# Kernel tuning notes

Measured on AMD Instinct MI355X. Metric: run time of the kernel, lower is better.

## Reference

```python
import jax, jax.numpy as jnp
import numpy as np

B, S, D, H, DK, DV = 2, 2048, 1024, 16, 64, 64
EPS = 1e-6

def setup_inputs() -> dict:
    key = jax.random.key(0)
    ks = jax.random.split(key, 5)
    sc = 1.0 / np.sqrt(D)
    return {
        "ip": jax.random.normal(ks[0], (B, S, D), jnp.float32),
        "wk": jax.random.normal(ks[1], (D, H * DK), jnp.float32) * sc,
        "wq": jax.random.normal(ks[2], (D, H * DK), jnp.float32) * sc,
        "wv": jax.random.normal(ks[3], (D, H * DV), jnp.float32) * sc,
        "fc_w": jax.random.normal(ks[4], (H * DV, D), jnp.float32) * (1.0 / np.sqrt(H * DV)),
        "fc_b": jnp.zeros((D,), jnp.float32),
        "ln_g": jnp.ones((D,), jnp.float32),
        "ln_b": jnp.zeros((D,), jnp.float32),
    }

def reference(ip, wk, wq, wv, fc_w, fc_b, ln_g, ln_b):
    m, t, _ = ip.shape
    temp = jnp.asarray(DK ** 0.5, ip.dtype)
    # projections -> [m, t, H, d]
    k = (ip @ wk).reshape(m, t, H, DK)
    q = (ip @ wq).reshape(m, t, H, DK)
    v = (ip @ wv).reshape(m, t, H, DV)
    # scores [m, H, t, t]; dropout is identity in eval mode
    scores = jnp.einsum('mqhd,mkhd->mhqk', q, k) / temp
    attn = jax.nn.softmax(scores, axis=-1)
    # context [m, t, H*DV]
    ctx = jnp.einsum('mhqk,mkhd->mqhd', attn, v).reshape(m, t, H * DV)
    out = ctx @ fc_w + fc_b + ip  # fc + residual
    # LayerNorm over last dim (biased variance, eps=1e-6)
    mu = jnp.mean(out, axis=-1, keepdims=True)
    var = jnp.mean(jnp.square(out - mu), axis=-1, keepdims=True)
    y = (out - mu) * jax.lax.rsqrt(var + EPS) * ln_g + ln_b
    return (y, attn)
```

## Files before the change

kernel.cpp:

```cpp
#include <hip/hip_runtime.h>
#include <hip/hip_bf16.h>
#include <stdint.h>

#define S_LEN 2048
#define DMODEL 1024
#define NH 16
#define HD 64
#define SC2 0.18033688011112042f

typedef __attribute__((ext_vector_type(8))) short bf16x8;
typedef __attribute__((ext_vector_type(4))) float f32x4;
typedef unsigned long long u64;

__device__ __forceinline__ void gload16(const void* g, void* l) {
  __builtin_amdgcn_global_load_lds(
      reinterpret_cast<const __attribute__((address_space(1))) void*>(reinterpret_cast<uintptr_t>(g)),
      reinterpret_cast<__attribute__((address_space(3))) void*>(reinterpret_cast<uintptr_t>(l)),
      16, 0, 0);
}

__device__ __forceinline__ f32x4 mfma_bf16(bf16x8 a, bf16x8 b, f32x4 c) {
  return __builtin_amdgcn_mfma_f32_16x16x32_bf16(a, b, c, 0, 0, 0);
}

__device__ __forceinline__ unsigned short bfbits(float x) {
  __hip_bfloat16 h = __float2bfloat16(x);
  return *reinterpret_cast<unsigned short*>(&h);
}

__device__ __forceinline__ float asf(unsigned u) {
  union { unsigned u; float f; } c; c.u = u; return c.f;
}

__device__ __forceinline__ void wait_vm0_bar() {
  __builtin_amdgcn_sched_barrier(0);
  asm volatile("s_waitcnt vmcnt(0) lgkmcnt(0)" ::: "memory");
  __builtin_amdgcn_s_barrier();
  __builtin_amdgcn_sched_barrier(0);
}
__device__ __forceinline__ void wait_vm2_bar() {
  __builtin_amdgcn_sched_barrier(0);
  asm volatile("s_waitcnt vmcnt(2) lgkmcnt(0)" ::: "memory");
  __builtin_amdgcn_s_barrier();
  __builtin_amdgcn_sched_barrier(0);
}
__device__ __forceinline__ void wait_vm4_bar() {
  __builtin_amdgcn_sched_barrier(0);
  asm volatile("s_waitcnt vmcnt(4) lgkmcnt(0)" ::: "memory");
  __builtin_amdgcn_s_barrier();
  __builtin_amdgcn_sched_barrier(0);
}

__global__ __launch_bounds__(256) void k_prep(const float* __restrict__ ip,
                                              const float* __restrict__ wq,
                                              const float* __restrict__ wk,
                                              const float* __restrict__ wv,
                                              const float* __restrict__ fcw,
                                              __hip_bfloat16* __restrict__ ipb,
                                              __hip_bfloat16* __restrict__ wt_all,
                                              __hip_bfloat16* __restrict__ fct) {
  int bid = blockIdx.x;
  if (bid < 4096) {
    int i = (bid * 256 + threadIdx.x) * 4;
    f32x4 v = *(const f32x4*)(ip + i);
    u64 p = (u64)bfbits(v[0]) | ((u64)bfbits(v[1]) << 16) | ((u64)bfbits(v[2]) << 32)
          | ((u64)bfbits(v[3]) << 48);
    *reinterpret_cast<u64*>(ipb + i) = p;
    return;
  }
  bid -= 4096;
  const int z = bid >> 10, tile_id = bid & 1023;
  const float* src = (z == 0) ? wq : (z == 1) ? wk : (z == 2) ? wv : fcw;
  __hip_bfloat16* dst = (z == 3) ? fct : wt_all + (size_t)z * DMODEL * DMODEL;
  __shared__ float tile[32][33];
  const int nb = (tile_id & 31) * 32, kb = (tile_id >> 5) * 32;
  const int lx = threadIdx.x & 31, ly = threadIdx.x >> 5;
#pragma unroll
  for (int i = 0; i < 4; ++i)
    tile[ly + 8 * i][lx] = src[(size_t)(kb + ly + 8 * i) * DMODEL + nb + lx];
  __syncthreads();
#pragma unroll
  for (int i = 0; i < 4; ++i)
    dst[(size_t)(nb + ly + 8 * i) * DMODEL + kb + lx] = __float2bfloat16(tile[lx][ly + 8 * i]);
}

__global__ __launch_bounds__(1024) void k_transpose_v(const unsigned short* __restrict__ V,
                                                      unsigned short* __restrict__ Vt) {
  __shared__ unsigned short tile[32][33];
  const int bh = blockIdx.z;
  const int sb = blockIdx.x * 32, db = blockIdx.y * 32;
  const unsigned short* src = V + (size_t)bh * S_LEN * HD;
  unsigned short* dst = Vt + (size_t)bh * HD * S_LEN;
  tile[threadIdx.y][threadIdx.x] = src[(size_t)(sb + threadIdx.y) * HD + db + threadIdx.x];
  __syncthreads();
  dst[(size_t)(db + threadIdx.y) * S_LEN + sb + threadIdx.x] = tile[threadIdx.x][threadIdx.y];
}

template <int MODE>
__global__ __launch_bounds__(256) void k_gemm(const __hip_bfloat16* __restrict__ A,
                                              const __hip_bfloat16* __restrict__ Bt,
                                              __hip_bfloat16* __restrict__ Q,
                                              __hip_bfloat16* __restrict__ Kk,
                                              __hip_bfloat16* __restrict__ V,
                                              const float* __restrict__ ipf,
                                              const float* __restrict__ bias,
                                              float* __restrict__ preln) {
  __shared__ __align__(128) char lds[16384];
  char* Al = lds;
  char* Bl = lds + 8192;
  const int t = threadIdx.x;
  const int w = t >> 6, l = t & 63;
  const int g = l >> 4, lr = l & 15;
  const int cpx = gridDim.x >> 3;
  const int swz = (blockIdx.x & 7) * cpx + (blockIdx.x >> 3);
  const int bm = swz & 31;
  const int bn = swz >> 5;

  int sr0 = (w * 2 + 0) * 16 + (l >> 2);
  int sr1 = (w * 2 + 1) * 16 + (l >> 2);
  const int sc = (l & 3) * 16;
  const char* aSrc0 = (const char*)A + ((size_t)(bm * 128 + sr0)) * 2048 + (sc ^ (((sr0 >> 1) & 3) << 4));
  const char* aSrc1 = (const char*)A + ((size_t)(bm * 128 + sr1)) * 2048 + (sc ^ (((sr1 >> 1) & 3) << 4));
  const char* bSrc0 = (const char*)Bt + ((size_t)(bn * 128 + sr0)) * 2048 + (sc ^ (((sr0 >> 1) & 3) << 4));
  const char* bSrc1 = (const char*)Bt + ((size_t)(bn * 128 + sr1)) * 2048 + (sc ^ (((sr1 >> 1) & 3) << 4));

  const int wm = (w >> 1) * 64, wn = (w & 1) * 64;
  int roff[4], noff[4];
#pragma unroll
  for (int mi = 0; mi < 4; ++mi) {
    int m = wm + mi * 16 + lr;
    roff[mi] = m * 64 + ((g * 16) ^ (((m >> 1) & 3) << 4));
  }
#pragma unroll
  for (int ni = 0; ni < 4; ++ni) {
    int n = wn + ni * 16 + lr;
    noff[ni] = n * 64 + ((g * 16) ^ (((n >> 1) & 3) << 4));
  }

  f32x4 acc[4][4] = {};
  for (int k0 = 0; k0 < DMODEL; k0 += 32) {
    gload16(aSrc0 + k0 * 2, Al + (w * 2 + 0) * 1024);
    gload16(aSrc1 + k0 * 2, Al + (w * 2 + 1) * 1024);
    gload16(bSrc0 + k0 * 2, Bl + (w * 2 + 0) * 1024);
    gload16(bSrc1 + k0 * 2, Bl + (w * 2 + 1) * 1024);
    __syncthreads();
    bf16x8 af[4], bfv[4];
#pragma unroll
    for (int mi = 0; mi < 4; ++mi) af[mi] = *(const bf16x8*)(Al + roff[mi]);
#pragma unroll
    for (int ni = 0; ni < 4; ++ni) bfv[ni] = *(const bf16x8*)(Bl + noff[ni]);
#pragma unroll
    for (int mi = 0; mi < 4; ++mi)
#pragma unroll
      for (int ni = 0; ni < 4; ++ni)
        acc[mi][ni] = mfma_bf16(af[mi], bfv[ni], acc[mi][ni]);
    __syncthreads();
  }

#pragma unroll
  for (int mi = 0; mi < 4; ++mi)
#pragma unroll
    for (int ni = 0; ni < 4; ++ni) {
      f32x4 v = acc[mi][ni];
#pragma unroll
      for (int r = 0; r < 4; ++r) {
        int m = bm * 128 + wm + mi * 16 + g * 4 + r;
        int n = bn * 128 + wn + ni * 16 + lr;
        if (MODE == 0) {
          int mat = n >> 10, c = n & 1023;
          int h = c >> 6, d = c & 63;
          int b = m >> 11, s = m & 2047;
          size_t idx = (((size_t)(b * NH + h)) * S_LEN + s) * HD + d;
          __hip_bfloat16 hv = __float2bfloat16(v[r]);
          if (mat == 0) Q[idx] = hv;
          else if (mat == 1) Kk[idx] = hv;
          else V[idx] = hv;
        } else {
          size_t idx = (size_t)m * DMODEL + n;
          preln[idx] = v[r] + bias[n] + ipf[idx];
        }
      }
    }
}

__global__ __launch_bounds__(256, 2) void k_attn8(const __hip_bfloat16* __restrict__ Q,
                                                  const __hip_bfloat16* __restrict__ K,
                                                  const __hip_bfloat16* __restrict__ Vt,
                                                  float* __restrict__ attn,
                                                  __hip_bfloat16* __restrict__ ctx) {
  __shared__ __align__(128) char KVst[4][8192];
  __shared__ __align__(128) char Pw[2][4][4096];

  const int t = threadIdx.x, w = t >> 6, l = t & 63;
  const int g = l >> 4, lr = l & 15;
  const int bid = blockIdx.x;
  const int bh = bid & 31, qi = bid >> 5;
  const int b = bh >> 4, h = bh & 15;
  const int q0 = qi * 64 + w * 16;
  const char* Kh = (const char*)(K + (size_t)bh * S_LEN * HD);
  const char* Vh = (const char*)(Vt + (size_t)bh * HD * S_LEN);
  const __hip_bfloat16* Qh = Q + (size_t)bh * S_LEN * HD;

  bf16x8 qf0 = *(const bf16x8*)(Qh + (size_t)(q0 + lr) * HD + 8 * g);
  bf16x8 qf1 = *(const bf16x8*)(Qh + (size_t)(q0 + lr) * HD + 32 + 8 * g);

  const int srow0 = w * 8 + (l >> 3), srow1 = srow0 + 32;
  const int sb = (l & 7) * 16;
  const int kso0 = srow0 * 128 + (sb ^ ((srow0 & 7) << 4));
  const int kso1 = srow1 * 128 + (sb ^ ((srow1 & 7) << 4));
  const int vso0 = srow0 * 4096 + (sb ^ ((srow0 & 7) << 4));
  const int vso1 = srow1 * 4096 + (sb ^ ((srow1 & 7) << 4));
  const int swz = (lr & 7) << 4;

  gload16(Kh + kso0, &KVst[0][w * 1024]);
  gload16(Kh + kso1, &KVst[0][4096 + w * 1024]);
  gload16(Kh + 8192 + kso0, &KVst[1][w * 1024]);
  gload16(Kh + 8192 + kso1, &KVst[1][4096 + w * 1024]);
  float lsum = 0.f;
#define P1_COMPUTE(c)                                                              \
  {                                                                                \
    const char* kb_ = &KVst[(c) & 3][0];                                           \
    _Pragma("unroll") for (int st = 0; st < 4; ++st) {                             \
      const char* kr = kb_ + (st * 16 + lr) * 128;                                 \
      bf16x8 kf0 = *(const bf16x8*)(kr + ((g * 16) ^ swz));                        \
      bf16x8 kf1 = *(const bf16x8*)(kr + ((64 + g * 16) ^ swz));                   \
      f32x4 s = {};                                                                \
      s = mfma_bf16(kf0, qf0, s);                                                  \
      s = mfma_bf16(kf1, qf1, s);                                                  \
      lsum += __builtin_amdgcn_exp2f(s[0] * SC2) + __builtin_amdgcn_exp2f(s[1] * SC2) \
            + __builtin_amdgcn_exp2f(s[2] * SC2) + __builtin_amdgcn_exp2f(s[3] * SC2); \
    }                                                                              \
  }
  for (int c = 0; c < 30; ++c) {
    gload16(Kh + (c + 2) * 8192 + kso0, &KVst[(c + 2) & 3][w * 1024]);
    gload16(Kh + (c + 2) * 8192 + kso1, &KVst[(c + 2) & 3][4096 + w * 1024]);
    wait_vm4_bar();
    P1_COMPUTE(c);
  }
  wait_vm2_bar();
  P1_COMPUTE(30);
  wait_vm0_bar();
  P1_COMPUTE(31);
#undef P1_COMPUTE
  lsum += __shfl_xor(lsum, 16);
  lsum += __shfl_xor(lsum, 32);
  const float inv = 1.0f / lsum;

  gload16(Kh + kso0, &KVst[0][w * 1024]);
  gload16(Kh + kso1, &KVst[0][4096 + w * 1024]);
  gload16(Vh + vso0, &KVst[2][w * 1024]);
  gload16(Vh + vso1, &KVst[2][4096 + w * 1024]);
  wait_vm0_bar();

  f32x4 o[4] = {};
  const size_t arowbase = ((size_t)bh * S_LEN + q0) * S_LEN;
  const int sl_row = l >> 5, sl_col = l & 31;
  for (int c = 0; c < 32; ++c) {
    const int cur = c & 1;
    const int gbuf = (c >> 1) & 1;
    const int ce = c & 1;
    if (c < 31) {
      gload16(Kh + (c + 1) * 8192 + kso0, &KVst[cur ^ 1][w * 1024]);
      gload16(Kh + (c + 1) * 8192 + kso1, &KVst[cur ^ 1][4096 + w * 1024]);
      gload16(Vh + (c + 1) * 128 + vso0, &KVst[2 + (cur ^ 1)][w * 1024]);
      gload16(Vh + (c + 1) * 128 + vso1, &KVst[2 + (cur ^ 1)][4096 + w * 1024]);
    }
    if (c >= 2) {
      const char* psrc = &Pw[gbuf ^ 1][w][0];
      const int kvb = ((c >> 1) - 1) * 128;
#pragma unroll
      for (int i = 0; i < 4; ++i) {
        int row = ce * 8 + 2 * i + sl_row;
        u64 v = *reinterpret_cast<const u64*>(psrc + row * 256 + ((sl_col * 8) ^ ((row & 7) << 4)));
        unsigned lo = (unsigned)v, hi = (unsigned)(v >> 32);
        f32x4 pv;
        pv[0] = asf(lo << 16);
        pv[1] = asf(lo & 0xffff0000u);
        pv[2] = asf(hi << 16);
        pv[3] = asf(hi & 0xffff0000u);
        __builtin_nontemporal_store(pv, (f32x4*)(attn + arowbase + (size_t)row * S_LEN + kvb + sl_col * 4));
      }
    }
#pragma unroll
    for (int st = 0; st < 4; ++st) {
      const char* kr = &KVst[cur][(st * 16 + lr) * 128];
      bf16x8 kf0 = *(const bf16x8*)(kr + ((g * 16) ^ swz));
      bf16x8 kf1 = *(const bf16x8*)(kr + ((64 + g * 16) ^ swz));
      f32x4 s = {};
      s = mfma_bf16(kf0, qf0, s);
      s = mfma_bf16(kf1, qf1, s);
      float p0 = __builtin_amdgcn_exp2f(s[0] * SC2) * inv;
      float p1 = __builtin_amdgcn_exp2f(s[1] * SC2) * inv;
      float p2 = __builtin_amdgcn_exp2f(s[2] * SC2) * inv;
      float p3 = __builtin_amdgcn_exp2f(s[3] * SC2) * inv;
      u64 u = (u64)bfbits(p0) | ((u64)bfbits(p1) << 16) | ((u64)bfbits(p2) << 32)
            | ((u64)bfbits(p3) << 48);
      *reinterpret_cast<u64*>(&Pw[gbuf][w][lr * 256 + ((ce * 128 + st * 32 + g * 8) ^ swz)]) = u;
    }
#pragma unroll
    for (int ks = 0; ks < 2; ++ks) {
      bf16x8 pf = *(const bf16x8*)(&Pw[gbuf][w][lr * 256 + ((ce * 128 + ks * 64 + g * 16) ^ swz)]);
#pragma unroll
      for (int dvt = 0; dvt < 4; ++dvt) {
        const char* vb = &KVst[2 + cur][(dvt * 16 + lr) * 128];
        bf16x8 vf = *(const bf16x8*)(vb + ((ks * 64 + g * 16) ^ swz));
        o[dvt] = mfma_bf16(pf, vf, o[dvt]);
      }
    }
    if (c < 31) wait_vm4_bar();
  }

  {
    const char* psrc = &Pw[1][w][0];
#pragma unroll
    for (int i = 0; i < 8; ++i) {
      int row = 2 * i + sl_row;
      u64 v = *reinterpret_cast<const u64*>(psrc + row * 256 + ((sl_col * 8) ^ ((row & 7) << 4)));
      unsigned lo = (unsigned)v, hi = (unsigned)(v >> 32);
      f32x4 pv;
      pv[0] = asf(lo << 16);
      pv[1] = asf(lo & 0xffff0000u);
      pv[2] = asf(hi << 16);
      pv[3] = asf(hi & 0xffff0000u);
      __builtin_nontemporal_store(pv, (f32x4*)(attn + arowbase + (size_t)row * S_LEN + 1920 + sl_col * 4));
    }
  }

#pragma unroll
  for (int dvt = 0; dvt < 4; ++dvt)
#pragma unroll
    for (int r = 0; r < 4; ++r) {
      int q = q0 + g * 4 + r;
      size_t idx = ((size_t)b * S_LEN + q) * DMODEL + h * HD + dvt * 16 + lr;
      ctx[idx] = __float2bfloat16(o[dvt][r]);
    }
}

__global__ __launch_bounds__(256) void k_ln(const float* __restrict__ x,
                                            const float* __restrict__ gam,
                                            const float* __restrict__ bet,
                                            float* __restrict__ y) {
  const int row = blockIdx.x;
  const int i = threadIdx.x * 4;
  const float* xr = x + (size_t)row * DMODEL;
  f32x4 v = *(const f32x4*)(xr + i);
  float s = v[0] + v[1] + v[2] + v[3];
  float s2 = v[0] * v[0] + v[1] * v[1] + v[2] * v[2] + v[3] * v[3];
#pragma unroll
  for (int off = 1; off < 64; off <<= 1) {
    s += __shfl_xor(s, off);
    s2 += __shfl_xor(s2, off);
  }
  __shared__ float red[2][4];
  const int w = threadIdx.x >> 6, ln = threadIdx.x & 63;
  if (ln == 0) { red[0][w] = s; red[1][w] = s2; }
  __syncthreads();
  s = red[0][0] + red[0][1] + red[0][2] + red[0][3];
  s2 = red[1][0] + red[1][1] + red[1][2] + red[1][3];
  const float mu = s * (1.f / DMODEL);
  const float rstd = rsqrtf(s2 * (1.f / DMODEL) - mu * mu + 1e-6f);
  f32x4 gv = *(const f32x4*)(gam + i), bv = *(const f32x4*)(bet + i);
  f32x4 out;
#pragma unroll
  for (int j = 0; j < 4; ++j) out[j] = (v[j] - mu) * rstd * gv[j] + bv[j];
  *(f32x4*)(y + (size_t)row * DMODEL + i) = out;
}

extern "C" void kernel_launch(void* const* d_in, const int* in_sizes, int n_in,
                              void* d_out, int out_size, void* d_ws, size_t ws_size,
                              hipStream_t stream) {
  const float* ip  = (const float*)d_in[0];
  const float* wk  = (const float*)d_in[1];
  const float* wq  = (const float*)d_in[2];
  const float* wv  = (const float*)d_in[3];
  const float* fcw = (const float*)d_in[4];
  const float* fcb = (const float*)d_in[5];
  const float* lng = (const float*)d_in[6];
  const float* lnb = (const float*)d_in[7];

  float* y = (float*)d_out;
  float* attn = y + (size_t)2 * S_LEN * DMODEL;

  char* ws = (char*)d_ws;
  __hip_bfloat16* ipb = (__hip_bfloat16*)(ws);
  __hip_bfloat16* wt  = (__hip_bfloat16*)(ws + (8ll << 20));
  __hip_bfloat16* fct = (__hip_bfloat16*)(ws + (14ll << 20));
  __hip_bfloat16* Qb  = (__hip_bfloat16*)(ws + (16ll << 20));
  __hip_bfloat16* Kb  = (__hip_bfloat16*)(ws + (24ll << 20));
  __hip_bfloat16* Vb  = (__hip_bfloat16*)(ws + (32ll << 20));
  __hip_bfloat16* Vtb = (__hip_bfloat16*)(ws + (40ll << 20));
  __hip_bfloat16* ctx = (__hip_bfloat16*)(ws + (48ll << 20));
  float* preln        = (float*)(ws + (56ll << 20));

  k_prep<<<8192, 256, 0, stream>>>(ip, wq, wk, wv, fcw, ipb, wt, fct);
  k_gemm<0><<<32 * 24, 256, 0, stream>>>(ipb, wt, Qb, Kb, Vb, nullptr, nullptr, nullptr);
  k_transpose_v<<<dim3(64, 2, 32), dim3(32, 32), 0, stream>>>((const unsigned short*)Vb,
                                                              (unsigned short*)Vtb);
  k_attn8<<<1024, 256, 0, stream>>>(Qb, Kb, Vtb, attn, ctx);
  k_gemm<1><<<32 * 8, 256, 0, stream>>>(ctx, fct, nullptr, nullptr, nullptr, ip, fcb, preln);
  k_ln<<<4096, 256, 0, stream>>>(preln, lng, lnb, y);
}
```

Measured before the change: 217.8 us.

## Fuse V transpose into QKV GEMM epilogue, read bf16 residual, raise MFMA priority

The QKV projection GEMM now writes V directly in transposed [bh, d, s] layout, packing four consecutive sequence elements into one 64-bit store. This removes the separate k_transpose_v kernel and its extra round trip through global memory. The output-projection GEMM reads the residual from the bf16 copy of the input instead of the fp32 original, halving that read but losing residual precision. The attention kernel also raises wave priority around the P·V MFMA block to favour matrix work over other waves.

New measurement: 211.8 us, median of 2. 2.8% less time.

```diff
diff --git a/kernel.cpp b/kernel.cpp
--- a/kernel.cpp
+++ b/kernel.cpp
@@ -84,25 +84,13 @@
     dst[(size_t)(nb + ly + 8 * i) * DMODEL + kb + lx] = __float2bfloat16(tile[lx][ly + 8 * i]);
 }
 
-__global__ __launch_bounds__(1024) void k_transpose_v(const unsigned short* __restrict__ V,
-                                                      unsigned short* __restrict__ Vt) {
-  __shared__ unsigned short tile[32][33];
-  const int bh = blockIdx.z;
-  const int sb = blockIdx.x * 32, db = blockIdx.y * 32;
-  const unsigned short* src = V + (size_t)bh * S_LEN * HD;
-  unsigned short* dst = Vt + (size_t)bh * HD * S_LEN;
-  tile[threadIdx.y][threadIdx.x] = src[(size_t)(sb + threadIdx.y) * HD + db + threadIdx.x];
-  __syncthreads();
-  dst[(size_t)(db + threadIdx.y) * S_LEN + sb + threadIdx.x] = tile[threadIdx.x][threadIdx.y];
-}
-
 template <int MODE>
 __global__ __launch_bounds__(256) void k_gemm(const __hip_bfloat16* __restrict__ A,
                                               const __hip_bfloat16* __restrict__ Bt,
                                               __hip_bfloat16* __restrict__ Q,
                                               __hip_bfloat16* __restrict__ Kk,
-                                              __hip_bfloat16* __restrict__ V,
-                                              const float* __restrict__ ipf,
+                                              __hip_bfloat16* __restrict__ Vt,
+                                              const __hip_bfloat16* __restrict__ resid,
                                               const float* __restrict__ bias,
                                               float* __restrict__ preln) {
   __shared__ __align__(128) char lds[16384];
@@ -162,22 +150,27 @@
 #pragma unroll
     for (int ni = 0; ni < 4; ++ni) {
       f32x4 v = acc[mi][ni];
-#pragma unroll
-      for (int r = 0; r < 4; ++r) {
-        int m = bm * 128 + wm + mi * 16 + g * 4 + r;
-        int n = bn * 128 + wn + ni * 16 + lr;
-        if (MODE == 0) {
-          int mat = n >> 10, c = n & 1023;
-          int h = c >> 6, d = c & 63;
-          int b = m >> 11, s = m & 2047;
-          size_t idx = (((size_t)(b * NH + h)) * S_LEN + s) * HD + d;
-          __hip_bfloat16 hv = __float2bfloat16(v[r]);
-          if (mat == 0) Q[idx] = hv;
-          else if (mat == 1) Kk[idx] = hv;
-          else V[idx] = hv;
+      const int m0 = bm * 128 + wm + mi * 16 + g * 4;
+      const int n = bn * 128 + wn + ni * 16 + lr;
+      if (MODE == 0) {
+        const int mat = n >> 10, c = n & 1023;
+        const int h = c >> 6, d = c & 63;
+        const int b = m0 >> 11, s0 = m0 & 2047;
+        if (mat == 2) {
+          u64 p = (u64)bfbits(v[0]) | ((u64)bfbits(v[1]) << 16) | ((u64)bfbits(v[2]) << 32)
+                | ((u64)bfbits(v[3]) << 48);
+          *reinterpret_cast<u64*>(Vt + ((size_t)(b * NH + h) * HD + d) * S_LEN + s0) = p;
         } else {
-          size_t idx = (size_t)m * DMODEL + n;
-          preln[idx] = v[r] + bias[n] + ipf[idx];
+          __hip_bfloat16* dst = (mat == 0) ? Q : Kk;
+#pragma unroll
+          for (int r = 0; r < 4; ++r)
+            dst[(((size_t)(b * NH + h)) * S_LEN + s0 + r) * HD + d] = __float2bfloat16(v[r]);
+        }
+      } else {
+#pragma unroll
+        for (int r = 0; r < 4; ++r) {
+          size_t idx = (size_t)(m0 + r) * DMODEL + n;
+          preln[idx] = v[r] + bias[n] + __bfloat162float(resid[idx]);
         }
       }
     }
@@ -297,6 +290,7 @@
             | ((u64)bfbits(p3) << 48);
       *reinterpret_cast<u64*>(&Pw[gbuf][w][lr * 256 + ((ce * 128 + st * 32 + g * 8) ^ swz)]) = u;
     }
+    __builtin_amdgcn_s_setprio(1);
 #pragma unroll
     for (int ks = 0; ks < 2; ++ks) {
       bf16x8 pf = *(const bf16x8*)(&Pw[gbuf][w][lr * 256 + ((ce * 128 + ks * 64 + g * 16) ^ swz)]);
@@ -307,6 +301,7 @@
         o[dvt] = mfma_bf16(pf, vf, o[dvt]);
       }
     }
+    __builtin_amdgcn_s_setprio(0);
     if (c < 31) wait_vm4_bar();
   }
 
@@ -387,16 +382,13 @@
   __hip_bfloat16* fct = (__hip_bfloat16*)(ws + (14ll << 20));
   __hip_bfloat16* Qb  = (__hip_bfloat16*)(ws + (16ll << 20));
   __hip_bfloat16* Kb  = (__hip_bfloat16*)(ws + (24ll << 20));
-  __hip_bfloat16* Vb  = (__hip_bfloat16*)(ws + (32ll << 20));
   __hip_bfloat16* Vtb = (__hip_bfloat16*)(ws + (40ll << 20));
   __hip_bfloat16* ctx = (__hip_bfloat16*)(ws + (48ll << 20));
   float* preln        = (float*)(ws + (56ll << 20));
 
   k_prep<<<8192, 256, 0, stream>>>(ip, wq, wk, wv, fcw, ipb, wt, fct);
-  k_gemm<0><<<32 * 24, 256, 0, stream>>>(ipb, wt, Qb, Kb, Vb, nullptr, nullptr, nullptr);
-  k_transpose_v<<<dim3(64, 2, 32), dim3(32, 32), 0, stream>>>((const unsigned short*)Vb,
-                                                              (unsigned short*)Vtb);
+  k_gemm<0><<<32 * 24, 256, 0, stream>>>(ipb, wt, Qb, Kb, Vtb, nullptr, nullptr, nullptr);
   k_attn8<<<1024, 256, 0, stream>>>(Qb, Kb, Vtb, attn, ctx);
-  k_gemm<1><<<32 * 8, 256, 0, stream>>>(ctx, fct, nullptr, nullptr, nullptr, ip, fcb, preln);
+  k_gemm<1><<<32 * 8, 256, 0, stream>>>(ctx, fct, nullptr, nullptr, nullptr, ipb, fcb, preln);
   k_ln<<<4096, 256, 0, stream>>>(preln, lng, lnb, y);
 }
```
